# Optimization experiments

Measured on AMD Instinct MI355X. Metric: run time of the kernel, lower is better.

Reference implementation:

```python
import jax, jax.numpy as jnp
import numpy as np

S_MIN = 0.01
S_MAX = 36500.0
SEQ_LEN = 128
BATCH = 65536


def setup_inputs() -> dict:
    key = jax.random.key(0)
    k1, k2 = jax.random.split(key)
    # elapsed days: nonnegative floats; ratings: integers 1..4 stored as float
    t = jax.random.uniform(k1, (SEQ_LEN, BATCH), dtype=jnp.float32) * 30.0
    rating = jax.random.randint(k2, (SEQ_LEN, BATCH), 1, 5).astype(jnp.float32)
    inputs = jnp.stack([t, rating], axis=-1)  # [S, B, 2]
    w = jnp.array([0.4, 0.6, 2.4, 5.8, 4.93, 0.94, 0.86, 0.01, 1.49,
                   0.14, 0.94, 2.18, 0.05, 0.34, 1.26, 0.29, 2.61],
                  dtype=jnp.float32)
    return {"inputs": inputs, "w": w}


def _first_step(X, w):
    # state is all-zeros only on the first step (clamp keeps s >= S_MIN after)
    rating = X[:, 1]
    ridx = jnp.clip(rating.astype(jnp.int32) - 1, 0, 3)
    valid = (rating >= 1) & (rating <= 4)
    new_s = jnp.where(valid, w[ridx], 1.0)
    new_d = jnp.clip(w[4] - w[5] * (rating - 3.0), 1.0, 10.0)
    new_s = jnp.clip(new_s, S_MIN, S_MAX)
    return jnp.stack([new_s, new_d], axis=1)  # [B, 2]


def _step(w, state, X):
    s, d = state[:, 0], state[:, 1]
    t, rating = X[:, 0], X[:, 1]
    # power forgetting curve: r = (1 + t / (9 s))^-1
    r = 1.0 / (1.0 + t / (9.0 * s))
    hard_penalty = jnp.where(rating == 2, w[15], 1.0)
    easy_bonus = jnp.where(rating == 4, w[16], 1.0)
    s_success = s * (1.0 + jnp.exp(w[8]) * (11.0 - d) * jnp.power(s, -w[9])
                     * (jnp.exp((1.0 - r) * w[10]) - 1.0)
                     * hard_penalty * easy_bonus)
    s_failure = jnp.minimum(
        w[11] * jnp.power(d, -w[12]) * (jnp.power(s + 1.0, w[13]) - 1.0)
        * jnp.exp((1.0 - r) * w[14]),
        s)
    new_s = jnp.where(rating > 1.0, s_success, s_failure)
    new_d = d - w[6] * (rating - 3.0)
    new_d = w[7] * w[4] + (1.0 - w[7]) * new_d  # mean reversion to w[4]
    new_d = jnp.clip(new_d, 1.0, 10.0)
    new_s = jnp.clip(new_s, S_MIN, S_MAX)
    new_state = jnp.stack([new_s, new_d], axis=1)
    return new_state, new_state


def reference(inputs, w):
    state0 = _first_step(inputs[0], w)  # [B, 2]
    final_state, rest = jax.lax.scan(lambda st, X: _step(w, st, X),
                                     state0, inputs[1:])
    outputs = jnp.concatenate([state0[None], rest], axis=0)  # [S, B, 2]
    return outputs, final_state
```

## Files before the change

### kernel.cpp

```cpp
#include <hip/hip_runtime.h>

#define BATCH_N 65536
#define SEQ_N   128

typedef float v2f __attribute__((ext_vector_type(2)));

__global__ __launch_bounds__(256, 1) void fsrs_kernel(
    const v2f* __restrict__ in,
    const float* __restrict__ w,
    v2f*       __restrict__ out)
{
    const int b = blockIdx.x * 256 + threadIdx.x;

    const float w0 = w[0], w1 = w[1], w2 = w[2], w3 = w[3];
    const float w4 = w[4], w5 = w[5], w6 = w[6], w7 = w[7];
    const float w9 = w[9], w11 = w[11], w12 = w[12], w13 = w[13];
    const float w15 = w[15], w16 = w[16];
    constexpr float LOG2E = 1.44269504088896340736f;
    const float w8l  = w[8]  * LOG2E;
    const float w10l = w[10] * LOG2E;
    const float w14l = w[14] * LOG2E;
    const float omw7   = 1.0f - w7;
    const float omw7w6 = omw7 * w6;
    const float dc0    = w7 * w4 + 3.0f * omw7w6;

    const v2f* ip = in  + b;
    v2f*       op = out + b;

    float s = 0.01f;
    float dpre = 1.0f;

    v2f rawA[16], rawB[16];
    float tX[16], dX[16], mX[16];
    float tY[16], dY[16], mY[16];

    auto loadC = [&](v2f* raw, int base) {
#pragma unroll
        for (int i = 0; i < 16; ++i) raw[i] = ip[(base + i) * BATCH_N];
    };

    auto preRow = [&](v2f r, float* T, float* D, float* M, int i) {
        const float tt = r.x, rating = r.y;
        const float hb = (rating == 2.0f) ? w15
                       : ((rating == 4.0f) ? w16 : 1.0f);
        const float eh = (11.0f - dpre) * hb;
        const float m2 = w11 * __builtin_amdgcn_exp2f(
                             -w12 * __builtin_amdgcn_logf(dpre));
        M[i] = (rating > 1.0f) ? eh : -m2;
        const float nd = __builtin_fmaf(omw7, dpre,
                          __builtin_fmaf(-omw7w6, rating, dc0));
        dpre = fminf(fmaxf(nd, 1.0f), 10.0f);
        T[i] = tt;
        D[i] = dpre;
    };

    auto stepRow = [&](float tt, float ms, float dd, int row) {
        const bool  sel = ms > 0.0f;
        const float q   = __builtin_fmaf(9.0f, s, tt);
        const float omr = tt * __builtin_amdgcn_rcpf(q);
        const float x   = omr * (sel ? w10l : w14l);
        const float ls  = __builtin_amdgcn_logf(sel ? s : (s + 1.0f));
        const float aa  = sel ? __builtin_fmaf(-w9, ls, w8l) : (w13 * ls);
        const float u   = __builtin_amdgcn_exp2f(aa + x);
        const float v   = __builtin_amdgcn_exp2f(sel ? aa : x);
        const float m   = sel ? (ms * s) : (-ms);
        const float P   = (u - v) * m;
        const float su  = fminf(s + P, 36500.0f);
        const float fl  = fmaxf(fminf(P, s), 0.01f);
        s = sel ? su : fl;
        v2f o; o.x = s; o.y = dd;
        __builtin_nontemporal_store(o, &op[row * BATCH_N]);
    };

    auto preC = [&](const v2f* raw, float* T, float* D, float* M, int lo) {
#pragma unroll
        for (int i = 0; i < 16; ++i) {
            if (i < lo) continue;
            preRow(raw[i], T, D, M, i);
        }
    };

    auto fused = [&](const float* T, const float* D, const float* M,
                     int sb, int lo,
                     const v2f* rawSrc, float* T2, float* D2, float* M2,
                     bool doPre, v2f* rawDst, int lb, bool doLoad) {
#pragma unroll
        for (int i = 0; i < 16; ++i) {
            if (doLoad) rawDst[i] = ip[(lb + i) * BATCH_N];
            if (doPre)  preRow(rawSrc[i], T2, D2, M2, i);
            if (i >= lo) stepRow(T[i], M[i], D[i], sb + i);
        }
    };

    loadC(rawA, 0);
    loadC(rawB, 16);

    const float r0 = rawA[0].y;
    {
        const float d0 = fminf(fmaxf(
            __builtin_fmaf(-w5, r0 - 3.0f, w4), 1.0f), 10.0f);
        dpre = d0;
        tX[0] = rawA[0].x; dX[0] = d0; mX[0] = 1.0f;
    }
    preC(rawA, tX, dX, mX, 1);

    {
        const float wsel = (r0 < 2.5f) ? ((r0 < 1.5f) ? w0 : w1)
                                       : ((r0 < 3.5f) ? w2 : w3);
        const float ns = (r0 >= 1.0f && r0 <= 4.0f) ? wsel : 1.0f;
        s = fminf(fmaxf(ns, 0.01f), 36500.0f);
        v2f o; o.x = s; o.y = dX[0];
        __builtin_nontemporal_store(o, &op[0]);
    }

    fused(tX, dX, mX, 0, 1, rawB, tY, dY, mY, true, rawA, 32, true);

#pragma unroll 1
    for (int c = 0; c < 3; ++c) {
        fused(tY, dY, mY, 16 * (2 * c + 1), 0,
              rawA, tX, dX, mX, true, rawB, 16 * (2 * c + 3), true);
        fused(tX, dX, mX, 16 * (2 * c + 2), 0,
              rawB, tY, dY, mY, true, rawA, 16 * (2 * c + 4), c < 2);
    }

    fused(tY, dY, mY, 112, 0, rawA, tX, dX, mX, false, rawB, 0, false);

    {
        v2f o; o.x = s; o.y = dY[15];
        op[SEQ_N * BATCH_N] = o;
    }
}

extern "C" void kernel_launch(void* const* d_in, const int* in_sizes, int n_in,
                              void* d_out, int out_size, void* d_ws, size_t ws_size,
                              hipStream_t stream) {
    const v2f*   in = (const v2f*)d_in[0];
    const float* w  = (const float*)d_in[1];
    v2f* out = (v2f*)d_out;
    fsrs_kernel<<<BATCH_N / 256, 256, 0, stream>>>(in, w, out);
}
```

Measured before the change: 113.1 us.

## Split warps into producer and consumer roles with LDS handoff

Each block now handles 128 batch elements with 256 threads: the upper 128 threads load inputs and precompute the difficulty chain and multipliers, writing them to double-buffered shared memory, while the lower 128 threads run the serial stability recurrence and store outputs. Phases are separated by block barriers. The aim is to overlap the independent difficulty chain and global loads with the dependent stability chain across wavefronts instead of within one thread. In exchange, half the threads do the loads and half the compute, and the change adds LDS traffic plus nine barriers.

```diff
diff --git a/kernel.cpp b/kernel.cpp
--- a/kernel.cpp
+++ b/kernel.cpp
@@ -2,15 +2,23 @@
 
 #define BATCH_N 65536
 #define SEQ_N   128
+#define ELB     128
+#define NPH     9
 
 typedef float v2f __attribute__((ext_vector_type(2)));
 
-__global__ __launch_bounds__(256, 1) void fsrs_kernel(
+__global__ __launch_bounds__(256, 2) void fsrs_kernel(
     const v2f* __restrict__ in,
     const float* __restrict__ w,
     v2f*       __restrict__ out)
 {
-    const int b = blockIdx.x * 256 + threadIdx.x;
+    const int tid = threadIdx.x;
+    const int ew  = tid & (ELB - 1);
+    const int b   = blockIdx.x * ELB + ew;
+    const bool isProd = tid >= ELB;
+
+    __shared__ v2f   lTM[2][16][ELB];
+    __shared__ float lD [2][16][ELB];
 
     const float w0 = w[0], w1 = w[1], w2 = w[2], w3 = w[3];
     const float w4 = w[4], w5 = w[5], w6 = w[6], w7 = w[7];
@@ -27,106 +35,101 @@
     const v2f* ip = in  + b;
     v2f*       op = out + b;
 
-    float s = 0.01f;
+    v2f raw0[16], raw1[16];
     float dpre = 1.0f;
+    float s = 0.01f, dcur = 1.0f;
 
-    v2f rawA[16], rawB[16];
-    float tX[16], dX[16], mX[16];
-    float tY[16], dY[16], mY[16];
-
-    auto loadC = [&](v2f* raw, int base) {
+    if (isProd) {
 #pragma unroll
-        for (int i = 0; i < 16; ++i) raw[i] = ip[(base + i) * BATCH_N];
-    };
-
-    auto preRow = [&](v2f r, float* T, float* D, float* M, int i) {
-        const float tt = r.x, rating = r.y;
-        const float hb = (rating == 2.0f) ? w15
-                       : ((rating == 4.0f) ? w16 : 1.0f);
-        const float eh = (11.0f - dpre) * hb;
-        const float m2 = w11 * __builtin_amdgcn_exp2f(
-                             -w12 * __builtin_amdgcn_logf(dpre));
-        M[i] = (rating > 1.0f) ? eh : -m2;
-        const float nd = __builtin_fmaf(omw7, dpre,
-                          __builtin_fmaf(-omw7w6, rating, dc0));
-        dpre = fminf(fmaxf(nd, 1.0f), 10.0f);
-        T[i] = tt;
-        D[i] = dpre;
-    };
-
-    auto stepRow = [&](float tt, float ms, float dd, int row) {
-        const bool  sel = ms > 0.0f;
-        const float q   = __builtin_fmaf(9.0f, s, tt);
-        const float omr = tt * __builtin_amdgcn_rcpf(q);
-        const float x   = omr * (sel ? w10l : w14l);
-        const float ls  = __builtin_amdgcn_logf(sel ? s : (s + 1.0f));
-        const float aa  = sel ? __builtin_fmaf(-w9, ls, w8l) : (w13 * ls);
-        const float u   = __builtin_amdgcn_exp2f(aa + x);
-        const float v   = __builtin_amdgcn_exp2f(sel ? aa : x);
-        const float m   = sel ? (ms * s) : (-ms);
-        const float P   = (u - v) * m;
-        const float su  = fminf(s + P, 36500.0f);
-        const float fl  = fmaxf(fminf(P, s), 0.01f);
-        s = sel ? su : fl;
-        v2f o; o.x = s; o.y = dd;
-        __builtin_nontemporal_store(o, &op[row * BATCH_N]);
-    };
-
-    auto preC = [&](const v2f* raw, float* T, float* D, float* M, int lo) {
+        for (int i = 0; i < 16; ++i) raw0[i] = ip[i * BATCH_N];
 #pragma unroll
-        for (int i = 0; i < 16; ++i) {
-            if (i < lo) continue;
-            preRow(raw[i], T, D, M, i);
-        }
-    };
-
-    auto fused = [&](const float* T, const float* D, const float* M,
-                     int sb, int lo,
-                     const v2f* rawSrc, float* T2, float* D2, float* M2,
-                     bool doPre, v2f* rawDst, int lb, bool doLoad) {
-#pragma unroll
-        for (int i = 0; i < 16; ++i) {
-            if (doLoad) rawDst[i] = ip[(lb + i) * BATCH_N];
-            if (doPre)  preRow(rawSrc[i], T2, D2, M2, i);
-            if (i >= lo) stepRow(T[i], M[i], D[i], sb + i);
-        }
-    };
-
-    loadC(rawA, 0);
-    loadC(rawB, 16);
-
-    const float r0 = rawA[0].y;
-    {
-        const float d0 = fminf(fmaxf(
-            __builtin_fmaf(-w5, r0 - 3.0f, w4), 1.0f), 10.0f);
-        dpre = d0;
-        tX[0] = rawA[0].x; dX[0] = d0; mX[0] = 1.0f;
-    }
-    preC(rawA, tX, dX, mX, 1);
-
-    {
-        const float wsel = (r0 < 2.5f) ? ((r0 < 1.5f) ? w0 : w1)
-                                       : ((r0 < 3.5f) ? w2 : w3);
-        const float ns = (r0 >= 1.0f && r0 <= 4.0f) ? wsel : 1.0f;
-        s = fminf(fmaxf(ns, 0.01f), 36500.0f);
-        v2f o; o.x = s; o.y = dX[0];
-        __builtin_nontemporal_store(o, &op[0]);
+        for (int i = 0; i < 16; ++i) raw1[i] = ip[(16 + i) * BATCH_N];
     }
 
-    fused(tX, dX, mX, 0, 1, rawB, tY, dY, mY, true, rawA, 32, true);
-
-#pragma unroll 1
-    for (int c = 0; c < 3; ++c) {
-        fused(tY, dY, mY, 16 * (2 * c + 1), 0,
-              rawA, tX, dX, mX, true, rawB, 16 * (2 * c + 3), true);
-        fused(tX, dX, mX, 16 * (2 * c + 2), 0,
-              rawB, tY, dY, mY, true, rawA, 16 * (2 * c + 4), c < 2);
+#pragma unroll
+    for (int p = 0; p < NPH; ++p) {
+        if (isProd && p < 8) {
+            const int par = p & 1;
+            v2f* rw = par ? raw1 : raw0;
+            int i0 = 0;
+            if (p == 0) {
+                const float t0 = rw[0].x, r0 = rw[0].y;
+                const float d0 = fminf(fmaxf(
+                    __builtin_fmaf(-w5, r0 - 3.0f, w4), 1.0f), 10.0f);
+                dpre = d0;
+                v2f tm; tm.x = t0; tm.y = r0;
+                lTM[0][0][ew] = tm;
+                lD [0][0][ew] = d0;
+                rw[0] = ip[32 * BATCH_N];
+                i0 = 1;
+            }
+#pragma unroll
+            for (int i = 0; i < 16; ++i) {
+                if (i < i0) continue;
+                const float tt = rw[i].x, rating = rw[i].y;
+                const float hb = (rating == 2.0f) ? w15
+                               : ((rating == 4.0f) ? w16 : 1.0f);
+                const float eh = (11.0f - dpre) * hb;
+                const float m2 = w11 * __builtin_amdgcn_exp2f(
+                                     -w12 * __builtin_amdgcn_logf(dpre));
+                const float M  = (rating > 1.0f) ? eh : -m2;
+                const float nd = __builtin_fmaf(omw7, dpre,
+                                  __builtin_fmaf(-omw7w6, rating, dc0));
+                dpre = fminf(fmaxf(nd, 1.0f), 10.0f);
+                v2f tm; tm.x = tt; tm.y = M;
+                lTM[par][i][ew] = tm;
+                lD [par][i][ew] = dpre;
+                if (p < 6) rw[i] = ip[((p + 2) * 16 + i) * BATCH_N];
+            }
+        }
+        if (!isProd && p >= 1) {
+            const int k   = p - 1;
+            const int par = k & 1;
+            int i0 = 0;
+            if (p == 1) {
+                const v2f tm0 = lTM[0][0][ew];
+                const float r0 = tm0.y;
+                const float wsel = (r0 < 2.5f) ? ((r0 < 1.5f) ? w0 : w1)
+                                               : ((r0 < 3.5f) ? w2 : w3);
+                const float ns = (r0 >= 1.0f && r0 <= 4.0f) ? wsel : 1.0f;
+                s = fminf(fmaxf(ns, 0.01f), 36500.0f);
+                dcur = lD[0][0][ew];
+                v2f o; o.x = s; o.y = dcur;
+                __builtin_nontemporal_store(o, &op[0]);
+                i0 = 1;
+            }
+#pragma unroll
+            for (int i = 0; i < 16; ++i) {
+                if (i < i0) continue;
+                const v2f  tm = lTM[par][i][ew];
+                const float dd = lD[par][i][ew];
+                const float tt = tm.x, ms = tm.y;
+                const bool  sel = ms > 0.0f;
+                const float q   = __builtin_fmaf(9.0f, s, tt);
+                const float omr = tt * __builtin_amdgcn_rcpf(q);
+                const float x   = omr * (sel ? w10l : w14l);
+                const float ls  = __builtin_amdgcn_logf(sel ? s : (s + 1.0f));
+                const float aa  = sel ? __builtin_fmaf(-w9, ls, w8l)
+                                      : (w13 * ls);
+                const float u   = __builtin_amdgcn_exp2f(aa + x);
+                const float v   = __builtin_amdgcn_exp2f(sel ? aa : x);
+                const float m   = sel ? (ms * s) : (-ms);
+                const float P   = (u - v) * m;
+                const float su  = fminf(s + P, 36500.0f);
+                const float fl  = fmaxf(fminf(P, s), 0.01f);
+                s = sel ? su : fl;
+                dcur = dd;
+                v2f o; o.x = s; o.y = dcur;
+                __builtin_nontemporal_store(o, &op[(k * 16 + i) * BATCH_N]);
+            }
+        }
+        asm volatile("s_waitcnt lgkmcnt(0)" ::: "memory");
+        __builtin_amdgcn_s_barrier();
+        asm volatile("" ::: "memory");
     }
 
-    fused(tY, dY, mY, 112, 0, rawA, tX, dX, mX, false, rawB, 0, false);
-
-    {
-        v2f o; o.x = s; o.y = dY[15];
+    if (!isProd) {
+        v2f o; o.x = s; o.y = dcur;
         op[SEQ_N * BATCH_N] = o;
     }
 }
@@ -137,5 +140,5 @@
     const v2f*   in = (const v2f*)d_in[0];
     const float* w  = (const float*)d_in[1];
     v2f* out = (v2f*)d_out;
-    fsrs_kernel<<<BATCH_N / 256, 256, 0, stream>>>(in, w, out);
+    fsrs_kernel<<<BATCH_N / ELB, 256, 0, stream>>>(in, w, out);
 }
```

After: 116.5 us. 3.0% more time.
